# Kernel tuning notes

Measured on AMD Instinct MI355X. Metric: run time of the kernel, lower is better.

The kernel has to match this reference:

```python
import jax, jax.numpy as jnp
import numpy as np


def setup_inputs() -> dict:
    key = jax.random.key(0)
    k1, k2 = jax.random.split(key)
    z = jax.random.normal(k1, (16, 256, 4096), dtype=jnp.float32)  # (B, z_dim, T)
    embedding = jax.random.normal(k2, (1024, 256), dtype=jnp.float32)  # (z_num, z_dim)
    return {"z": z, "embedding": embedding}


def reference(z, embedding):
    # z: (B, C, T) -> (B, T, C), matching z.transpose(1, 2)
    zt = jnp.transpose(z, (0, 2, 1))
    B, T, C = zt.shape
    z_flat = zt.reshape(-1, C)  # (N, C), N = B*T

    # squared-euclidean distances: ||z||^2 + ||e||^2 - 2 z e^T  -> (N, K)
    distances = (
        jnp.sum(z_flat * z_flat, axis=1, keepdims=True)
        + jnp.sum(embedding * embedding, axis=1)
        - 2.0 * z_flat @ embedding.T
    )
    encoding_idx = jnp.argmin(distances, axis=1)  # (N,)
    z_vq = embedding[encoding_idx].reshape(B, T, C)

    # perplexity of code usage (one-hot scatter -> mean)
    K = embedding.shape[0]
    counts = jnp.zeros((K,), dtype=jnp.float32).at[encoding_idx].add(1.0)
    avg_probs = counts / encoding_idx.shape[0]
    perplexity = jnp.exp(-jnp.sum(avg_probs * jnp.log(avg_probs + 1e-10)))

    # sparsity = cross_entropy(E E^T, arange) = mean(logsumexp(row) - diag)
    logits = embedding @ embedding.T  # (K, K)
    sparsity = jnp.mean(jax.nn.logsumexp(logits, axis=1) - jnp.diag(logits))

    sg = jax.lax.stop_gradient
    z_qut_loss = jnp.sum((z_vq - sg(zt)) ** 2)   # mse_loss reduction='sum'
    z_enc_loss = jnp.sum((sg(z_vq) - zt) ** 2)

    # straight-through estimator
    z_st = zt + sg(z_vq - zt)
    out = jnp.transpose(z_st, (0, 2, 1))  # back to (B, C, T)
    return (out, z_qut_loss, z_enc_loss, perplexity, sparsity)
```

## Files before the change

kernel.cpp:

```cpp
#include <hip/hip_runtime.h>
#include <math.h>

typedef unsigned int u32;
typedef unsigned long long u64;
typedef _Float16 f16x8 __attribute__((ext_vector_type(8)));
typedef _Float16 f16x4 __attribute__((ext_vector_type(4)));
typedef float f32x4 __attribute__((ext_vector_type(4)));
typedef __attribute__((address_space(1))) const char gch;
typedef __attribute__((address_space(3))) char lch;

#define ZD 256
#define KC 1024
#define TT 4096
#define BB 16
#define NROWS (BB*TT)
#define TAU 0.12f
#define FLAGCAP 32768

__device__ __forceinline__ u32 flip32(float s) {
    int i = __float_as_int(s);
    return (u32)(i ^ ((i >> 31) | 0x80000000));
}
__device__ __forceinline__ float unflip32(u32 u) {
    int m = (~(((int)u) >> 31)) | 0x80000000;
    return __int_as_float((int)(u ^ (u32)m));
}

__global__ __launch_bounds__(256)
void vq_prep_kernel(const float* __restrict__ emb, _Float16* __restrict__ eh,
                    float* __restrict__ re, int* __restrict__ cnt) {
    int gid = blockIdx.x * 256 + threadIdx.x;
    if (gid < 2) cnt[gid] = 0;

    int code = gid >> 6;
    int lane = threadIdx.x & 63;
    float4 v = *(const float4*)(emb + (size_t)code * ZD + lane * 4);
    float s = v.x*v.x + v.y*v.y + v.z*v.z + v.w*v.w;
    #pragma unroll
    for (int off = 32; off; off >>= 1) s += __shfl_down(s, off, 64);
    if (lane == 0) re[code] = s;

    f16x4 hv;
    hv[0] = (_Float16)v.x; hv[1] = (_Float16)v.y;
    hv[2] = (_Float16)v.z; hv[3] = (_Float16)v.w;
    *(f16x4*)(eh + (size_t)code * ZD + lane * 4) = hv;
}

__device__ __forceinline__ void stage_half4(const char* ehc, char* dstbase,
                                            int h, int w, int l) {
    const int srow = h * 16384;
    #pragma unroll
    for (int j = 0; j < 4; ++j) {
        const int gi  = w * 4 + j;
        const int c   = 2 * gi + (l >> 5);
        const int kbs = (l & 31) * 16;
        const int off = srow + c * 512 + (kbs ^ ((c & 7) << 4));
        __builtin_amdgcn_global_load_lds((gch*)(ehc + off),
                                         (lch*)(dstbase + gi * 1024), 16, 0, 0);
    }
}

__device__ __forceinline__ void compute_phase32(const char* hb, int h,
                                                const f16x8 (&ah)[2][8], const float* reL,
                                                float (&v1)[8], float (&v2)[8], int (&i1)[8],
                                                int lane15, int lk) {
    #pragma unroll
    for (int cg = 0; cg < 2; ++cg) {
        const int c  = cg * 16 + lane15;
        const int sw = (lane15 & 7) << 4;
        f16x8 bh[8];
        #pragma unroll
        for (int ks = 0; ks < 8; ++ks)
            bh[ks] = *(const f16x8*)(hb + c * 512 + ((lk * 16 + ks * 64) ^ sw));

        f32x4 a0 = {0.f, 0.f, 0.f, 0.f};
        f32x4 a1 = {0.f, 0.f, 0.f, 0.f};
        __builtin_amdgcn_s_setprio(1);
        #pragma unroll
        for (int ks = 0; ks < 8; ++ks) {
            a0 = __builtin_amdgcn_mfma_f32_16x16x32_f16(ah[0][ks], bh[ks], a0, 0, 0, 0);
            a1 = __builtin_amdgcn_mfma_f32_16x16x32_f16(ah[1][ks], bh[ks], a1, 0, 0, 0);
        }
        __builtin_amdgcn_s_setprio(0);

        const int codeg = h * 32 + c;
        const float rc = reL[codeg];
        #pragma unroll
        for (int r = 0; r < 4; ++r) {
            float s0 = fmaf(-2.f, a0[r], rc);
            float n2a = fminf(fmaxf(v1[r], s0), v2[r]);
            i1[r] = (s0 < v1[r]) ? codeg : i1[r];
            v1[r] = fminf(v1[r], s0);
            v2[r] = n2a;
            float s1 = fmaf(-2.f, a1[r], rc);
            float n2b = fminf(fmaxf(v1[4 + r], s1), v2[4 + r]);
            i1[4 + r] = (s1 < v1[4 + r]) ? codeg : i1[4 + r];
            v1[4 + r] = fminf(v1[4 + r], s1);
            v2[4 + r] = n2b;
        }
    }
}

__global__ __launch_bounds__(256, 2)
void vq_argmin_mfma(const float* __restrict__ z, const _Float16* __restrict__ eh,
                    const float* __restrict__ emb, const float* __restrict__ re,
                    float* __restrict__ out, float* __restrict__ lossP,
                    int* __restrict__ idx, int* __restrict__ cnt,
                    int* __restrict__ flags) {
    __shared__ __align__(16) char lds[71168];
    float* reL   = (float*)(lds + 65536);
    float* zsqL  = (float*)(lds + 69632);
    int*   idsL  = (int*)  (lds + 70144);
    float* lossL = (float*)(lds + 70656);

    const int tid = threadIdx.x;
    const int w   = tid >> 6;
    const int l   = tid & 63;
    const int lane15 = l & 15;
    const int lk     = l >> 4;
    const int r0  = blockIdx.x * 128;
    const int b   = r0 >> 12;
    const int t0  = r0 & 4095;
    const char* ehc = (const char*)eh;

    *(float4*)(reL + tid * 4) = *(const float4*)(re + tid * 4);

    f16x8 ah[2][8];
    float zsq[2] = {0.f, 0.f};
    {
        const char* zb = (const char*)(z + (size_t)b * ZD * TT + t0 + w * 32);
        char* zdst = lds + w * 16384;
        #pragma unroll
        for (int round = 0; round < 2; ++round) {
            #pragma unroll
            for (int j = 0; j < 16; ++j) {
                const int c  = round * 128 + j * 8 + (l >> 3);
                const int tb = (l & 7) * 16;
                const char* src = zb + (size_t)c * TT * 4 + tb;
                __builtin_amdgcn_global_load_lds((gch*)src, (lch*)(zdst + j * 1024),
                                                 16, 0, 0);
            }
            asm volatile("s_waitcnt vmcnt(0)" ::: "memory");
            __builtin_amdgcn_sched_barrier(0);
            #pragma unroll
            for (int rg = 0; rg < 2; ++rg) {
                const int tw = rg * 16 + lane15;
                #pragma unroll
                for (int ks2 = 0; ks2 < 4; ++ks2) {
                    const int cl = ks2 * 32 + lk * 8;
                    f16x8 h;
                    #pragma unroll
                    for (int j = 0; j < 8; ++j) {
                        float v = *(const float*)(zdst + (cl + j) * 128 + tw * 4);
                        zsq[rg] = fmaf(v, v, zsq[rg]);
                        h[j] = (_Float16)v;
                    }
                    ah[rg][round * 4 + ks2] = h;
                }
            }
            asm volatile("s_waitcnt lgkmcnt(0)" ::: "memory");
            __builtin_amdgcn_sched_barrier(0);
        }
    }
    #pragma unroll
    for (int rg = 0; rg < 2; ++rg) {
        zsq[rg] += __shfl_xor(zsq[rg], 16, 64);
        zsq[rg] += __shfl_xor(zsq[rg], 32, 64);
        if (l < 16) zsqL[w * 32 + rg * 16 + l] = zsq[rg];
    }

    float v1[8], v2[8];
    int   i1[8];
    #pragma unroll
    for (int s8 = 0; s8 < 8; ++s8) { v1[s8] = 3.4e38f; v2[s8] = 3.4e38f; i1[s8] = 0; }

    asm volatile("s_waitcnt vmcnt(0) lgkmcnt(0)" ::: "memory");
    __syncthreads();
    stage_half4(ehc, lds,         0, w, l);
    stage_half4(ehc, lds + 16384, 1, w, l);
    stage_half4(ehc, lds + 32768, 2, w, l);

    for (int h = 0; h < 30; ++h) {
        asm volatile("s_waitcnt vmcnt(8)" ::: "memory");
        __builtin_amdgcn_sched_barrier(0);
        __builtin_amdgcn_s_barrier();
        if (h < 29) stage_half4(ehc, lds + ((h + 3) & 3) * 16384, h + 3, w, l);
        compute_phase32(lds + (h & 3) * 16384, h, ah, reL, v1, v2, i1, lane15, lk);
    }
    asm volatile("s_waitcnt vmcnt(4)" ::: "memory");
    __builtin_amdgcn_sched_barrier(0);
    __builtin_amdgcn_s_barrier();
    compute_phase32(lds + (30 & 3) * 16384, 30, ah, reL, v1, v2, i1, lane15, lk);
    asm volatile("s_waitcnt vmcnt(0)" ::: "memory");
    __builtin_amdgcn_sched_barrier(0);
    __builtin_amdgcn_s_barrier();
    compute_phase32(lds + (31 & 3) * 16384, 31, ah, reL, v1, v2, i1, lane15, lk);

    #pragma unroll
    for (int off = 1; off < 16; off <<= 1) {
        #pragma unroll
        for (int s8 = 0; s8 < 8; ++s8) {
            float ov1 = __shfl_xor(v1[s8], off, 64);
            int   oi1 = __shfl_xor(i1[s8], off, 64);
            float ov2 = __shfl_xor(v2[s8], off, 64);
            float nv2 = fminf(fmaxf(v1[s8], ov1), fminf(v2[s8], ov2));
            if (ov1 < v1[s8] || (ov1 == v1[s8] && oi1 < i1[s8])) { v1[s8] = ov1; i1[s8] = oi1; }
            v2[s8] = nv2;
        }
    }
    if (lane15 == 0) {
        #pragma unroll
        for (int s8 = 0; s8 < 8; ++s8) {
            const int rg = s8 >> 2, rr = s8 & 3;
            const int row = w * 32 + rg * 16 + lk * 4 + rr;
            idsL[row] = i1[s8];
            const bool fl = (v2[s8] - v1[s8] < TAU);
            lossL[row] = fl ? zsqL[row] : (zsqL[row] + v1[s8]);
            if (fl) {
                int p = atomicAdd(cnt, 1);
                if (p < FLAGCAP) flags[p] = (r0 + row) | (i1[s8] << 16);
            }
        }
    }
    __syncthreads();

    if (tid < 128) {
        idx[r0 + tid] = idsL[tid];
        float lv = lossL[tid];
        #pragma unroll
        for (int off = 32; off; off >>= 1) lv += __shfl_down(lv, off, 64);
        if (l == 0) zsqL[tid >> 6] = lv;
    }
    __syncthreads();
    if (tid == 0) lossP[blockIdx.x] = zsqL[0] + zsqL[1];

    {
        const int c0 = w * 64;
        float* ob = out + (size_t)b * ZD * TT + t0;
        #pragma unroll
        for (int half = 0; half < 2; ++half) {
            const int tt = half * 64 + l;
            const int ii = idsL[tt];
            const float4* er4 = (const float4*)(emb + (size_t)ii * ZD + c0);
            #pragma unroll
            for (int c4 = 0; c4 < 16; ++c4) {
                float4 ev = er4[c4];
                float* o0 = ob + (size_t)(c0 + c4 * 4) * TT + tt;
                o0[0]      = ev.x;
                o0[TT]     = ev.y;
                o0[2 * TT] = ev.z;
                o0[3 * TT] = ev.w;
            }
        }
    }
}

__global__ __launch_bounds__(256)
void vq_fixup_spar(const float* __restrict__ z, const float* __restrict__ emb,
                   const float* __restrict__ re, const int* __restrict__ cnt,
                   const int* __restrict__ flags, float* __restrict__ out,
                   int* __restrict__ idx, float* __restrict__ spar,
                   float* __restrict__ addP) {
    const int tid = threadIdx.x;
    const int w   = tid >> 6;
    const int lane = tid & 63;

    if (blockIdx.x >= 128) {
        __shared__ __align__(16) float er[8][260];
        __shared__ float wmaxS[8][4];
        __shared__ float wsumS[8][4];
        __shared__ float shD[8];
        const int bid2 = blockIdx.x - 128;
        const int r0   = bid2 * 8;

        for (int i = tid; i < 8 * 256; i += 256) er[i >> 8][i & 255] = emb[(size_t)r0 * ZD + i];
        __syncthreads();

        float dots[4][8];
        #pragma unroll
        for (int cc = 0; cc < 4; ++cc) {
            const int c = cc * 256 + tid;
            const float4* ec = (const float4*)(emb + (size_t)c * ZD);
            float a[8] = {0.f,0.f,0.f,0.f,0.f,0.f,0.f,0.f};
            for (int k4 = 0; k4 < ZD / 4; ++k4) {
                float4 e4 = ec[k4];
                #pragma unroll
                for (int r = 0; r < 8; ++r) {
                    const float* a4 = &er[r][k4 * 4];
                    a[r] = fmaf(e4.x, a4[0], fmaf(e4.y, a4[1],
                           fmaf(e4.z, a4[2], fmaf(e4.w, a4[3], a[r]))));
                }
            }
            #pragma unroll
            for (int r = 0; r < 8; ++r) dots[cc][r] = a[r];
            const int gr = c - r0;
            if (gr >= 0 && gr < 8) shD[gr] = a[gr];
        }
        #pragma unroll
        for (int r = 0; r < 8; ++r) {
            float m = fmaxf(fmaxf(dots[0][r], dots[1][r]), fmaxf(dots[2][r], dots[3][r]));
            #pragma unroll
            for (int off = 32; off; off >>= 1) m = fmaxf(m, __shfl_xor(m, off, 64));
            if (lane == 0) wmaxS[r][w] = m;
        }
        __syncthreads();
        #pragma unroll
        for (int r = 0; r < 8; ++r) {
            const float M = fmaxf(fmaxf(wmaxS[r][0], wmaxS[r][1]),
                                  fmaxf(wmaxS[r][2], wmaxS[r][3]));
            float se = expf(dots[0][r] - M) + expf(dots[1][r] - M)
                     + expf(dots[2][r] - M) + expf(dots[3][r] - M);
            #pragma unroll
            for (int off = 32; off; off >>= 1) se += __shfl_xor(se, off, 64);
            if (lane == 0) wsumS[r][w] = se;
        }
        __syncthreads();
        if (tid == 0) {
            float acc = 0.f;
            #pragma unroll
            for (int r = 0; r < 8; ++r) {
                const float M = fmaxf(fmaxf(wmaxS[r][0], wmaxS[r][1]),
                                      fmaxf(wmaxS[r][2], wmaxS[r][3]));
                const float S = wsumS[r][0] + wsumS[r][1] + wsumS[r][2] + wsumS[r][3];
                acc += M + logf(S) - shD[r];
            }
            spar[bid2] = acc;
        }
        return;
    }

    __shared__ __align__(16) float zs[8][ZD];
    __shared__ u64 sb[4][8];
    __shared__ int nwS[8];
    __shared__ float addS;
    int n = cnt[0];
    if (n > FLAGCAP) n = FLAGCAP;
    float blkLoss = 0.f;

    for (int base = blockIdx.x * 8; base < n; base += 128 * 8) {
        const int nr = (n - base < 8) ? (n - base) : 8;
        __syncthreads();
        for (int i = tid; i < nr * 256; i += 256) {
            const int r = i >> 8, k = i & 255;
            const int rowg = flags[base + r] & 0xFFFF;
            zs[r][k] = z[(size_t)(rowg >> 12) * ZD * TT + (size_t)k * TT + (rowg & 4095)];
        }
        __syncthreads();

        u64 best[8];
        #pragma unroll
        for (int r = 0; r < 8; ++r) best[r] = 0xFFFFFFFFFFFFFFFFull;

        for (int cc = 0; cc < 4; ++cc) {
            const int c = cc * 256 + tid;
            const float4* ec = (const float4*)(emb + (size_t)c * ZD);
            float a[8] = {0.f,0.f,0.f,0.f,0.f,0.f,0.f,0.f};
            for (int k4 = 0; k4 < ZD / 4; ++k4) {
                float4 e4 = ec[k4];
                #pragma unroll
                for (int r = 0; r < 8; ++r) {
                    const float* a4 = &zs[r][k4 * 4];
                    a[r] = fmaf(e4.x, a4[0], fmaf(e4.y, a4[1],
                           fmaf(e4.z, a4[2], fmaf(e4.w, a4[3], a[r]))));
                }
            }
            const float rc = re[c];
            #pragma unroll
            for (int r = 0; r < 8; ++r) {
                if (r < nr) {
                    float s = fmaf(-2.f, a[r], rc);
                    u64 pk = ((u64)flip32(s) << 32) | (u32)c;
                    if (pk < best[r]) best[r] = pk;
                }
            }
        }
        #pragma unroll
        for (int r = 0; r < 8; ++r) {
            if (r < nr) {
                u64 bv = best[r];
                #pragma unroll
                for (int off = 32; off; off >>= 1) {
                    u64 o = (u64)__shfl_xor((long long)bv, off, 64);
                    if (o < bv) bv = o;
                }
                if (lane == 0) sb[w][r] = bv;
            }
        }
        __syncthreads();
        if (tid == 0) addS = 0.f;
        __syncthreads();
        if (tid < nr) {
            u64 m = sb[0][tid];
            if (sb[1][tid] < m) m = sb[1][tid];
            if (sb[2][tid] < m) m = sb[2][tid];
            if (sb[3][tid] < m) m = sb[3][tid];
            const int nc  = (int)(u32)(m & 0xFFFFFFFFull);
            const float s = unflip32((u32)(m >> 32));
            const int rowg = flags[base + tid] & 0xFFFF;
            const int old  = (flags[base + tid] >> 16) & 1023;
            atomicAdd(&addS, s);
            if (nc != old) { idx[rowg] = nc; nwS[tid] = nc; }
            else nwS[tid] = -1;
        }
        __syncthreads();
        if (tid == 0) blkLoss += addS;
        for (int r = 0; r < nr; ++r) {
            const int nw = nwS[r];
            if (nw >= 0) {
                const int rowg = flags[base + r] & 0xFFFF;
                out[(size_t)(rowg >> 12) * ZD * TT + (size_t)tid * TT + (rowg & 4095)]
                    = emb[(size_t)nw * ZD + tid];
            }
        }
    }
    if (tid == 0) addP[blockIdx.x] = blkLoss;
}

__global__ __launch_bounds__(1024)
void vq_final_kernel(const int* __restrict__ idx, const float* __restrict__ spar,
                     const float* __restrict__ lossP, const float* __restrict__ addP,
                     float* __restrict__ scal) {
    __shared__ int   histL[4][1024];
    __shared__ float red[1024];
    const int tid = threadIdx.x;
    const int g   = tid >> 8;

    #pragma unroll
    for (int j = 0; j < 4; ++j) histL[j][tid & 255 | ((tid >> 8) << 8)] = 0;
    histL[0][tid] = 0; histL[1][tid] = 0; histL[2][tid] = 0; histL[3][tid] = 0;
    __syncthreads();
    #pragma unroll 4
    for (int i = 0; i < 64; ++i)
        atomicAdd(&histL[g][idx[i * 1024 + tid]], 1);
    __syncthreads();
    const int hc = histL[0][tid] + histL[1][tid] + histL[2][tid] + histL[3][tid];
    float p = (float)hc * (1.0f / (float)NROWS);
    red[tid] = -p * logf(p + 1e-10f);
    __syncthreads();
    for (int st = 512; st; st >>= 1) {
        if (tid < st) red[tid] += red[tid + st];
        __syncthreads();
    }
    if (tid == 0) scal[2] = expf(red[0]);
    __syncthreads();

    red[tid] = (tid < 512 ? lossP[tid] : 0.f) + ((tid < 128) ? addP[tid] : 0.f);
    __syncthreads();
    for (int st = 512; st; st >>= 1) {
        if (tid < st) red[tid] += red[tid + st];
        __syncthreads();
    }
    if (tid == 0) { scal[0] = red[0]; scal[1] = red[0]; }
    __syncthreads();

    red[tid] = (tid < 128) ? spar[tid] : 0.f;
    __syncthreads();
    for (int st = 512; st; st >>= 1) {
        if (tid < st) red[tid] += red[tid + st];
        __syncthreads();
    }
    if (tid == 0) scal[3] = red[0] * (1.0f / (float)KC);
}

extern "C" void kernel_launch(void* const* d_in, const int* in_sizes, int n_in,
                              void* d_out, int out_size, void* d_ws, size_t ws_size,
                              hipStream_t stream) {
    const float* z   = (const float*)d_in[0];
    const float* emb = (const float*)d_in[1];
    float* out = (float*)d_out;
    const size_t NOUT = (size_t)BB * ZD * TT;
    float* scal = out + NOUT;

    float* re    = (float*)d_ws;
    int*   cnt   = (int*)(re + KC);
    int*   flags = cnt + 4;
    float* spar  = (float*)(flags + FLAGCAP);
    float* lossP = spar + 128;
    float* addP  = lossP + 512;
    int*   idx   = (int*)(addP + 128);
    _Float16* eh = (_Float16*)(idx + NROWS);

    vq_prep_kernel<<<256, 256, 0, stream>>>(emb, eh, re, cnt);
    vq_argmin_mfma<<<NROWS / 128, 256, 0, stream>>>(z, eh, emb, re, out, lossP, idx,
                                                    cnt, flags);
    vq_fixup_spar<<<256, 256, 0, stream>>>(z, emb, re, cnt, flags, out, idx, spar, addP);
    vq_final_kernel<<<1, 1024, 0, stream>>>(idx, spar, lossP, addP, scal);
}
```

Baseline: 169.9 us.

## Shrink LDS footprint to fit three blocks per CU with triple-buffered codebook staging

Cuts the argmin kernel's shared memory from about 71KB to 53KB so three workgroups can reside per CU, and raises launch bounds to match. The codebook pipeline drops from four 16KB buffers to three, so prefetch depth falls from three stages to two. The z tile staging now runs in four rounds of 8KB per wave. Per-row squared norms move from LDS into registers via shuffles, and the loss reduction becomes a per-wave shuffle reduction. Higher occupancy is meant to hide latency, at the cost of a shallower prefetch and possible register pressure under the tighter launch bound.

```diff
diff --git a/kernel.cpp b/kernel.cpp
--- a/kernel.cpp
+++ b/kernel.cpp
@@ -101,17 +101,16 @@
     }
 }
 
-__global__ __launch_bounds__(256, 2)
+__global__ __launch_bounds__(256, 3)
 void vq_argmin_mfma(const float* __restrict__ z, const _Float16* __restrict__ eh,
                     const float* __restrict__ emb, const float* __restrict__ re,
                     float* __restrict__ out, float* __restrict__ lossP,
                     int* __restrict__ idx, int* __restrict__ cnt,
                     int* __restrict__ flags) {
-    __shared__ __align__(16) char lds[71168];
-    float* reL   = (float*)(lds + 65536);
-    float* zsqL  = (float*)(lds + 69632);
-    int*   idsL  = (int*)  (lds + 70144);
-    float* lossL = (float*)(lds + 70656);
+    __shared__ __align__(16) char lds[53248];
+    float* reL    = (float*)(lds + 49152);
+    int*   idsL   = (int*)lds;
+    float* wlossL = (float*)(lds + 512);
 
     const int tid = threadIdx.x;
     const int w   = tid >> 6;
@@ -129,12 +128,12 @@
     float zsq[2] = {0.f, 0.f};
     {
         const char* zb = (const char*)(z + (size_t)b * ZD * TT + t0 + w * 32);
-        char* zdst = lds + w * 16384;
-        #pragma unroll
-        for (int round = 0; round < 2; ++round) {
-            #pragma unroll
-            for (int j = 0; j < 16; ++j) {
-                const int c  = round * 128 + j * 8 + (l >> 3);
+        char* zdst = lds + w * 8192;
+        #pragma unroll
+        for (int round = 0; round < 4; ++round) {
+            #pragma unroll
+            for (int j = 0; j < 8; ++j) {
+                const int c  = round * 64 + j * 8 + (l >> 3);
                 const int tb = (l & 7) * 16;
                 const char* src = zb + (size_t)c * TT * 4 + tb;
                 __builtin_amdgcn_global_load_lds((gch*)src, (lch*)(zdst + j * 1024),
@@ -146,7 +145,7 @@
             for (int rg = 0; rg < 2; ++rg) {
                 const int tw = rg * 16 + lane15;
                 #pragma unroll
-                for (int ks2 = 0; ks2 < 4; ++ks2) {
+                for (int ks2 = 0; ks2 < 2; ++ks2) {
                     const int cl = ks2 * 32 + lk * 8;
                     f16x8 h;
                     #pragma unroll
@@ -155,7 +154,7 @@
                         zsq[rg] = fmaf(v, v, zsq[rg]);
                         h[j] = (_Float16)v;
                     }
-                    ah[rg][round * 4 + ks2] = h;
+                    ah[rg][round * 2 + ks2] = h;
                 }
             }
             asm volatile("s_waitcnt lgkmcnt(0)" ::: "memory");
@@ -166,7 +165,6 @@
     for (int rg = 0; rg < 2; ++rg) {
         zsq[rg] += __shfl_xor(zsq[rg], 16, 64);
         zsq[rg] += __shfl_xor(zsq[rg], 32, 64);
-        if (l < 16) zsqL[w * 32 + rg * 16 + l] = zsq[rg];
     }
 
     float v1[8], v2[8];
@@ -178,23 +176,18 @@
     __syncthreads();
     stage_half4(ehc, lds,         0, w, l);
     stage_half4(ehc, lds + 16384, 1, w, l);
-    stage_half4(ehc, lds + 32768, 2, w, l);
-
-    for (int h = 0; h < 30; ++h) {
-        asm volatile("s_waitcnt vmcnt(8)" ::: "memory");
+
+    for (int h = 0; h < 31; ++h) {
+        asm volatile("s_waitcnt vmcnt(4)" ::: "memory");
         __builtin_amdgcn_sched_barrier(0);
         __builtin_amdgcn_s_barrier();
-        if (h < 29) stage_half4(ehc, lds + ((h + 3) & 3) * 16384, h + 3, w, l);
-        compute_phase32(lds + (h & 3) * 16384, h, ah, reL, v1, v2, i1, lane15, lk);
-    }
-    asm volatile("s_waitcnt vmcnt(4)" ::: "memory");
-    __builtin_amdgcn_sched_barrier(0);
-    __builtin_amdgcn_s_barrier();
-    compute_phase32(lds + (30 & 3) * 16384, 30, ah, reL, v1, v2, i1, lane15, lk);
+        if (h < 30) stage_half4(ehc, lds + ((h + 2) % 3) * 16384, h + 2, w, l);
+        compute_phase32(lds + (h % 3) * 16384, h, ah, reL, v1, v2, i1, lane15, lk);
+    }
     asm volatile("s_waitcnt vmcnt(0)" ::: "memory");
     __builtin_amdgcn_sched_barrier(0);
     __builtin_amdgcn_s_barrier();
-    compute_phase32(lds + (31 & 3) * 16384, 31, ah, reL, v1, v2, i1, lane15, lk);
+    compute_phase32(lds + (31 % 3) * 16384, 31, ah, reL, v1, v2, i1, lane15, lk);
 
     #pragma unroll
     for (int off = 1; off < 16; off <<= 1) {
@@ -208,6 +201,16 @@
             v2[s8] = nv2;
         }
     }
+
+    float zsr[8];
+    #pragma unroll
+    for (int s8 = 0; s8 < 8; ++s8) {
+        const int rg = s8 >> 2, rr = s8 & 3;
+        zsr[s8] = __shfl(zsq[rg], lk * 4 + rr, 64);
+    }
+
+    __syncthreads();
+    float lossw = 0.f;
     if (lane15 == 0) {
         #pragma unroll
         for (int s8 = 0; s8 < 8; ++s8) {
@@ -215,24 +218,20 @@
             const int row = w * 32 + rg * 16 + lk * 4 + rr;
             idsL[row] = i1[s8];
             const bool fl = (v2[s8] - v1[s8] < TAU);
-            lossL[row] = fl ? zsqL[row] : (zsqL[row] + v1[s8]);
+            lossw += fl ? zsr[s8] : (zsr[s8] + v1[s8]);
             if (fl) {
                 int p = atomicAdd(cnt, 1);
                 if (p < FLAGCAP) flags[p] = (r0 + row) | (i1[s8] << 16);
             }
         }
     }
-    __syncthreads();
-
-    if (tid < 128) {
-        idx[r0 + tid] = idsL[tid];
-        float lv = lossL[tid];
-        #pragma unroll
-        for (int off = 32; off; off >>= 1) lv += __shfl_down(lv, off, 64);
-        if (l == 0) zsqL[tid >> 6] = lv;
-    }
-    __syncthreads();
-    if (tid == 0) lossP[blockIdx.x] = zsqL[0] + zsqL[1];
+    lossw += __shfl_xor(lossw, 16, 64);
+    lossw += __shfl_xor(lossw, 32, 64);
+    if (l == 0) wlossL[w] = lossw;
+    __syncthreads();
+
+    if (tid < 128) idx[r0 + tid] = idsL[tid];
+    if (tid == 0) lossP[blockIdx.x] = wlossL[0] + wlossL[1] + wlossL[2] + wlossL[3];
 
     {
         const int c0 = w * 64;
@@ -425,8 +424,6 @@
     const int tid = threadIdx.x;
     const int g   = tid >> 8;
 
-    #pragma unroll
-    for (int j = 0; j < 4; ++j) histL[j][tid & 255 | ((tid >> 8) << 8)] = 0;
     histL[0][tid] = 0; histL[1][tid] = 0; histL[2][tid] = 0; histL[3][tid] = 0;
     __syncthreads();
     #pragma unroll 4
```

After: 172.8 us. About the same (+1.7%).
